# Optimization experiments

Measured on AMD Instinct MI355X. Metric: run time of the kernel, lower is better.

The kernel has to match this reference:

```python
import math
import jax, jax.numpy as jnp
import numpy as np

B, T, N_EMBD, N_HEAD = 1, 16384, 1024, 1
N_ITERS = 30


def setup_inputs() -> dict:
    key = jax.random.key(0)
    kx, kw = jax.random.split(key)
    x = jax.random.normal(kx, (B, T, N_EMBD), dtype=jnp.float32)
    W = jax.random.normal(kw, (2 * N_EMBD + 1, N_EMBD), dtype=jnp.float32) * 0.02
    alpha = jnp.asarray(1.0, dtype=jnp.float32)  # nn.Parameter init
    beta = jnp.asarray(5.0, dtype=jnp.float32)   # nn.Parameter init
    return {"x": x, "W": W, "alpha": alpha, "beta": beta}


def _forward(x, W, alpha, beta):
    Bv, Tv, C = x.shape
    hd = C // N_HEAD
    qkv = x @ W.T                                            # (B,T,2C+1)
    q, k, v = qkv[..., :C], qkv[..., C:2 * C], qkv[..., 2 * C:]
    kh = k.reshape(Bv, Tv, N_HEAD, hd).transpose(0, 2, 1, 3)  # (B,H,T,hd)
    vh = v.reshape(Bv, Tv, N_HEAD, 1).transpose(0, 2, 1, 3)   # (B,H,T,1)
    q_last = q[:, -1].reshape(Bv, N_HEAD, hd)                 # last-token query
    scale = 0.001 / math.sqrt(hd)
    # Only the last query row of the causal attention matrix is consumed;
    # it attends all T keys (causal mask is all-ones on the last row).
    att = jnp.einsum('bhd,bhtd->bht', q_last, kh) * scale     # (B,H,T)
    att = att.at[:, :, -1].set(-jnp.inf)                      # exclude self key
    idx = jnp.arange(Tv)
    counts = (Tv - 1 - idx).astype(att.dtype)                 # distance from end

    def step(carry, _):
        a, b, k_old, done, p = carry
        kk = 2.0 * (a + b) / a                                # truncated window k = 2/p
        window = jnp.ceil(kk)
        mask = idx >= (Tv - window)                           # last `window` keys
        p_new = jax.nn.softmax(jnp.where(mask, att, -jnp.inf), axis=-1)
        bu = jnp.einsum('bht,t->', p_new, counts)             # beta_update (B=H=1 -> scalar)
        a_new, b_new = a + 1.0, b + bu
        done_new = done | (kk > Tv) | (kk < k_old)            # torch break conditions
        k_old_new = jax.lax.stop_gradient(kk)                 # k_old = k.detach()
        keep = lambda old, new: jnp.where(done, old, new)     # freeze after break
        return (keep(a, a_new), keep(b, b_new), keep(k_old, k_old_new),
                done_new, keep(p, p_new)), None

    init = (alpha.astype(att.dtype), beta.astype(att.dtype),
            jnp.asarray(0.0, att.dtype), jnp.asarray(False), jnp.zeros_like(att))
    (_, _, _, _, p), _ = jax.lax.scan(step, init, None, length=N_ITERS)
    # p is zero outside the final window, so the full-length contraction equals
    # att @ v[:, :, -window:, :].
    y = jnp.einsum('bht,bhtd->bhd', p, vh)
    return y.reshape(Bv, 1, 1)


def reference(x, W, alpha, beta):
    return _forward(x, W, alpha, beta)
```

## Files before the change

kernel.cpp:

```cpp
#include <hip/hip_runtime.h>
#include <math.h>

#define T_LEN 16384
#define C_DIM 1024
#define TAIL  256
#define SCAN_ITERS 30


__global__ __launch_bounds__(256)
void k_qw(const float* __restrict__ x, const float* __restrict__ W,
          float* __restrict__ partials) {
    const int tid = threadIdx.x, lane = tid & 63, wid = tid >> 6;
    const int blk = blockIdx.x;
    __shared__ float q_sh[4];

    const float4* xl = (const float4*)(x + (size_t)(T_LEN - 1) * C_DIM);
    const int row = blk * 4 + wid;
    const float4* wq = (const float4*)(W + (size_t)row * C_DIM);
    float acc = 0.f;
#pragma unroll
    for (int it = 0; it < 4; ++it) {
        int idx = lane + 64 * it;
        float4 a = wq[idx];
        float4 b = xl[idx];
        acc += a.x * b.x + a.y * b.y + a.z * b.z + a.w * b.w;
    }
#pragma unroll
    for (int off = 32; off > 0; off >>= 1) acc += __shfl_down(acc, off, 64);
    if (lane == 0) q_sh[wid] = acc;
    __syncthreads();

    const float* Wk = W + (size_t)C_DIM * C_DIM;
    float4 p4 = make_float4(0.f, 0.f, 0.f, 0.f);
#pragma unroll
    for (int r = 0; r < 4; ++r) {
        int ir = blk * 4 + r;
        float4 wkv = ((const float4*)(Wk + (size_t)ir * C_DIM))[tid];
        float qv = q_sh[r];
        p4.x += qv * wkv.x; p4.y += qv * wkv.y;
        p4.z += qv * wkv.z; p4.w += qv * wkv.w;
    }
    ((float4*)(partials + (size_t)blk * C_DIM))[tid] = p4;
}

__global__ __launch_bounds__(256)
void k_red(const float* __restrict__ partials, float* __restrict__ w_eff,
           unsigned int* __restrict__ cnt) {
    const int tid = threadIdx.x, blk = blockIdx.x;
    if (blk == 0 && tid == 0) cnt[0] = 0;
    __shared__ float sh[16][17];
    const int cl = tid & 15, seg = tid >> 4;
    const int col = blk * 16 + cl;
    float s = 0.f;
#pragma unroll
    for (int r = 0; r < 16; ++r)
        s += partials[(size_t)(seg * 16 + r) * C_DIM + col];
    sh[seg][cl] = s;
    __syncthreads();
    if (tid < 16) {
        float t2 = 0.f;
#pragma unroll
        for (int g = 0; g < 16; ++g) t2 += sh[g][tid];
        w_eff[blk * 16 + tid] = t2;
    }
}

__global__ __launch_bounds__(256)
void k_attv(const float* __restrict__ x, const float* __restrict__ W,
            const float* __restrict__ w_eff,
            const float* __restrict__ alpha_p, const float* __restrict__ beta_p,
            unsigned int* __restrict__ cnt,
            float* __restrict__ att, float* __restrict__ v,
            float* __restrict__ out) {
    const int tid = threadIdx.x, lane = tid & 63, wid = tid >> 6;
    const int blk = blockIdx.x;
    __shared__ float redA[4], redV[4];
    __shared__ float red4[4];
    __shared__ float totZ[4], totC[4], totV[4];
    __shared__ float sZ[TAIL], sV[TAIL], sBU[TAIL];
    __shared__ int   last_sh;

    {
        const int t = T_LEN - TAIL + blk;
        const float4* xr = (const float4*)(x + (size_t)t * C_DIM);
        const float4* we = (const float4*)w_eff;
        const float4* wv = (const float4*)(W + (size_t)(2 * C_DIM) * C_DIM);
        float4 a  = xr[tid];
        float4 e  = we[tid];
        float4 bv = wv[tid];
        float accA = a.x * e.x  + a.y * e.y  + a.z * e.z  + a.w * e.w;
        float accV = a.x * bv.x + a.y * bv.y + a.z * bv.z + a.w * bv.w;
#pragma unroll
        for (int off = 32; off > 0; off >>= 1) {
            accA += __shfl_down(accA, off, 64);
            accV += __shfl_down(accV, off, 64);
        }
        if (lane == 0) { redA[wid] = accA; redV[wid] = accV; }
        __syncthreads();
        if (tid == 0) {
            float A = redA[0] + redA[1] + redA[2] + redA[3];
            float V = redV[0] + redV[1] + redV[2] + redV[3];
            const float scale = (float)(0.001 / 32.0);
            att[blk] = (t == T_LEN - 1) ? -INFINITY : A * scale;
            v[blk]   = V;
        }
    }

    __syncthreads();
    if (tid == 0) {
        __threadfence();
        unsigned int ticket = atomicAdd(&cnt[0], 1u);
        last_sh = (ticket == 255u);
    }
    __syncthreads();
    if (!last_sh) return;
    __threadfence();

    const int u = TAIL - 1 - tid;
    const float av = att[u];
    const float vv = v[u];

    float m = av;
#pragma unroll
    for (int off = 32; off > 0; off >>= 1) m = fmaxf(m, __shfl_xor(m, off, 64));
    if (lane == 0) red4[wid] = m;
    __syncthreads();
    m = fmaxf(fmaxf(red4[0], red4[1]), fmaxf(red4[2], red4[3]));

    float e = expf(av - m);
    float c = e * (float)(TAIL - 1 - u);
    float w = e * vv;

    float pz = e, pc = c, pw = w;
#pragma unroll
    for (int off = 1; off < 64; off <<= 1) {
        float tz = __shfl_up(pz, off, 64);
        float tc = __shfl_up(pc, off, 64);
        float tw = __shfl_up(pw, off, 64);
        if (lane >= off) { pz += tz; pc += tc; pw += tw; }
    }
    if (lane == 63) { totZ[wid] = pz; totC[wid] = pc; totV[wid] = pw; }
    __syncthreads();
    {
        float az = 0.f, ac = 0.f, aw = 0.f;
        for (int w2 = 0; w2 < wid; ++w2) { az += totZ[w2]; ac += totC[w2]; aw += totV[w2]; }
        float Zu = pz + az;
        sZ[u]  = Zu;
        sV[u]  = pw + aw;
        sBU[u] = (pc + ac) / Zu;
    }
    __syncthreads();

    if (tid == 0) {
        float a = alpha_p[0], b = beta_p[0], k_old = 0.f;
        int f_start = 0;
        for (int it = 0; it < SCAN_ITERS; ++it) {
            float kk = 2.0f * (a + b) / a;
            float wf = ceilf(kk);
            int start;
            if (wf >= (float)TAIL) start = 0;
            else { int win = (int)wf; start = TAIL - win; if (start < 0) start = 0; }

            float bu = sBU[start];
            f_start = start;
            bool done_next = (kk > (float)T_LEN) || (kk < k_old);
            k_old = kk;
            a += 1.0f;
            b += bu;
            if (done_next) break;
        }
        out[0] = sV[f_start] / sZ[f_start];
    }
}

extern "C" void kernel_launch(void* const* d_in, const int* in_sizes, int n_in,
                              void* d_out, int out_size, void* d_ws, size_t ws_size,
                              hipStream_t stream) {
    const float* x     = (const float*)d_in[0];
    const float* W     = (const float*)d_in[1];
    const float* alpha = (const float*)d_in[2];
    const float* beta  = (const float*)d_in[3];

    float* ws         = (float*)d_ws;
    unsigned int* cnt = (unsigned int*)d_ws;
    float* w_eff      = ws + 16;
    float* att        = w_eff + C_DIM;
    float* v          = att + TAIL;
    float* partials   = v + TAIL;
    float* outp       = (float*)d_out;

    k_qw  <<<256, 256, 0, stream>>>(x, W, partials);
    k_red <<<64,  256, 0, stream>>>(partials, w_eff, cnt);
    k_attv<<<256, 256, 0, stream>>>(x, W, w_eff, alpha, beta, cnt, att, v, outp);
}
```

Baseline: 108.9 us.

## Fuse q/w_eff/attention kernels into one grid with redundant row-group recompute

```diff
diff --git a/kernel.cpp b/kernel.cpp
--- a/kernel.cpp
+++ b/kernel.cpp
@@ -5,104 +5,93 @@
 #define C_DIM 1024
 #define TAIL  256
 #define SCAN_ITERS 30
-
+#define NRG   32
+#define NTG   8
 
 __global__ __launch_bounds__(256)
-void k_qw(const float* __restrict__ x, const float* __restrict__ W,
-          float* __restrict__ partials) {
+void k_fused(const float* __restrict__ x, const float* __restrict__ W,
+             const float* __restrict__ alpha_p, const float* __restrict__ beta_p,
+             unsigned int* __restrict__ cnt,
+             float* __restrict__ attp, float* __restrict__ v,
+             float* __restrict__ out) {
     const int tid = threadIdx.x, lane = tid & 63, wid = tid >> 6;
     const int blk = blockIdx.x;
-    __shared__ float q_sh[4];
+    const int i = blk & 31;
+    const int j = blk >> 5;
+
+    __shared__ float  q_sh[32];
+    __shared__ float4 w_part4[256];
+    __shared__ float  red4[4];
+    __shared__ float  totZ[4], totC[4], totV[4];
+    __shared__ float  sZ[TAIL], sV[TAIL], sBU[TAIL];
+    __shared__ int    last_sh;
 
     const float4* xl = (const float4*)(x + (size_t)(T_LEN - 1) * C_DIM);
-    const int row = blk * 4 + wid;
-    const float4* wq = (const float4*)(W + (size_t)row * C_DIM);
-    float acc = 0.f;
+    float4 xv[4];
 #pragma unroll
-    for (int it = 0; it < 4; ++it) {
-        int idx = lane + 64 * it;
-        float4 a = wq[idx];
-        float4 b = xl[idx];
-        acc += a.x * b.x + a.y * b.y + a.z * b.z + a.w * b.w;
+    for (int it = 0; it < 4; ++it) xv[it] = xl[lane + 64 * it];
+
+    const int R0 = i * 32;
+#pragma unroll
+    for (int rr = 0; rr < 8; ++rr) {
+        const int row = R0 + wid * 8 + rr;
+        const float4* wq = (const float4*)(W + (size_t)row * C_DIM);
+        float acc = 0.f;
+#pragma unroll
+        for (int it = 0; it < 4; ++it) {
+            float4 a = wq[lane + 64 * it];
+            float4 b = xv[it];
+            acc += a.x * b.x + a.y * b.y + a.z * b.z + a.w * b.w;
+        }
+#pragma unroll
+        for (int off = 32; off > 0; off >>= 1) acc += __shfl_down(acc, off, 64);
+        if (lane == 0) q_sh[wid * 8 + rr] = acc;
     }
-#pragma unroll
-    for (int off = 32; off > 0; off >>= 1) acc += __shfl_down(acc, off, 64);
-    if (lane == 0) q_sh[wid] = acc;
     __syncthreads();
 
-    const float* Wk = W + (size_t)C_DIM * C_DIM;
-    float4 p4 = make_float4(0.f, 0.f, 0.f, 0.f);
+    {
+        const float* Wk = W + (size_t)C_DIM * C_DIM;
+        float4 wp = make_float4(0.f, 0.f, 0.f, 0.f);
 #pragma unroll
-    for (int r = 0; r < 4; ++r) {
-        int ir = blk * 4 + r;
-        float4 wkv = ((const float4*)(Wk + (size_t)ir * C_DIM))[tid];
-        float qv = q_sh[r];
-        p4.x += qv * wkv.x; p4.y += qv * wkv.y;
-        p4.z += qv * wkv.z; p4.w += qv * wkv.w;
+        for (int r = 0; r < 32; ++r) {
+            float4 kv = ((const float4*)(Wk + (size_t)(R0 + r) * C_DIM))[tid];
+            float qv = q_sh[r];
+            wp.x += qv * kv.x; wp.y += qv * kv.y;
+            wp.z += qv * kv.z; wp.w += qv * kv.w;
+        }
+        w_part4[tid] = wp;
     }
-    ((float4*)(partials + (size_t)blk * C_DIM))[tid] = p4;
-}
-
-__global__ __launch_bounds__(256)
-void k_red(const float* __restrict__ partials, float* __restrict__ w_eff,
-           unsigned int* __restrict__ cnt) {
-    const int tid = threadIdx.x, blk = blockIdx.x;
-    if (blk == 0 && tid == 0) cnt[0] = 0;
-    __shared__ float sh[16][17];
-    const int cl = tid & 15, seg = tid >> 4;
-    const int col = blk * 16 + cl;
-    float s = 0.f;
-#pragma unroll
-    for (int r = 0; r < 16; ++r)
-        s += partials[(size_t)(seg * 16 + r) * C_DIM + col];
-    sh[seg][cl] = s;
     __syncthreads();
-    if (tid < 16) {
-        float t2 = 0.f;
-#pragma unroll
-        for (int g = 0; g < 16; ++g) t2 += sh[g][tid];
-        w_eff[blk * 16 + tid] = t2;
-    }
-}
-
-__global__ __launch_bounds__(256)
-void k_attv(const float* __restrict__ x, const float* __restrict__ W,
-            const float* __restrict__ w_eff,
-            const float* __restrict__ alpha_p, const float* __restrict__ beta_p,
-            unsigned int* __restrict__ cnt,
-            float* __restrict__ att, float* __restrict__ v,
-            float* __restrict__ out) {
-    const int tid = threadIdx.x, lane = tid & 63, wid = tid >> 6;
-    const int blk = blockIdx.x;
-    __shared__ float redA[4], redV[4];
-    __shared__ float red4[4];
-    __shared__ float totZ[4], totC[4], totV[4];
-    __shared__ float sZ[TAIL], sV[TAIL], sBU[TAIL];
-    __shared__ int   last_sh;
 
     {
-        const int t = T_LEN - TAIL + blk;
-        const float4* xr = (const float4*)(x + (size_t)t * C_DIM);
-        const float4* we = (const float4*)w_eff;
+        const bool do_v = (i == 0);
         const float4* wv = (const float4*)(W + (size_t)(2 * C_DIM) * C_DIM);
-        float4 a  = xr[tid];
-        float4 e  = we[tid];
-        float4 bv = wv[tid];
-        float accA = a.x * e.x  + a.y * e.y  + a.z * e.z  + a.w * e.w;
-        float accV = a.x * bv.x + a.y * bv.y + a.z * bv.z + a.w * bv.w;
 #pragma unroll
-        for (int off = 32; off > 0; off >>= 1) {
-            accA += __shfl_down(accA, off, 64);
-            accV += __shfl_down(accV, off, 64);
-        }
-        if (lane == 0) { redA[wid] = accA; redV[wid] = accV; }
-        __syncthreads();
-        if (tid == 0) {
-            float A = redA[0] + redA[1] + redA[2] + redA[3];
-            float V = redV[0] + redV[1] + redV[2] + redV[3];
-            const float scale = (float)(0.001 / 32.0);
-            att[blk] = (t == T_LEN - 1) ? -INFINITY : A * scale;
-            v[blk]   = V;
+        for (int tt = 0; tt < 8; ++tt) {
+            const int tl = j * 32 + tt * 4 + wid;
+            const int t  = T_LEN - TAIL + tl;
+            const float4* xr = (const float4*)(x + (size_t)t * C_DIM);
+            float accA = 0.f, accV = 0.f;
+#pragma unroll
+            for (int it = 0; it < 4; ++it) {
+                const int idx = lane + 64 * it;
+                float4 a  = xr[idx];
+                float4 wp = w_part4[idx];
+                accA += a.x * wp.x + a.y * wp.y + a.z * wp.z + a.w * wp.w;
+                if (do_v) {
+                    float4 bv = wv[idx];
+                    accV += a.x * bv.x + a.y * bv.y + a.z * bv.z + a.w * bv.w;
+                }
+            }
+#pragma unroll
+            for (int off = 32; off > 0; off >>= 1) {
+                accA += __shfl_down(accA, off, 64);
+                if (do_v) accV += __shfl_down(accV, off, 64);
+            }
+            if (lane == 0) {
+                attp[(size_t)i * TAIL + tl] = accA;
+                if (do_v) v[tl] = accV;
+            }
         }
     }
 
@@ -110,14 +99,18 @@
     if (tid == 0) {
         __threadfence();
         unsigned int ticket = atomicAdd(&cnt[0], 1u);
-        last_sh = (ticket == 255u);
+        last_sh = (ticket == (NRG * NTG - 1));
     }
     __syncthreads();
     if (!last_sh) return;
     __threadfence();
 
     const int u = TAIL - 1 - tid;
-    const float av = att[u];
+    float s = 0.f;
+#pragma unroll
+    for (int k = 0; k < NRG; ++k) s += attp[(size_t)k * TAIL + u];
+    const float scale = (float)(0.001 / 32.0);
+    const float av = (u == TAIL - 1) ? -INFINITY : s * scale;
     const float vv = v[u];
 
     float m = av;
@@ -183,13 +176,11 @@
 
     float* ws         = (float*)d_ws;
     unsigned int* cnt = (unsigned int*)d_ws;
-    float* w_eff      = ws + 16;
-    float* att        = w_eff + C_DIM;
-    float* v          = att + TAIL;
-    float* partials   = v + TAIL;
+    float* attp       = ws + 16;
+    float* v          = attp + (size_t)NRG * TAIL;
     float* outp       = (float*)d_out;
 
-    k_qw  <<<256, 256, 0, stream>>>(x, W, partials);
-    k_red <<<64,  256, 0, stream>>>(partials, w_eff, cnt);
-    k_attv<<<256, 256, 0, stream>>>(x, W, w_eff, alpha, beta, cnt, att, v, outp);
+    hipMemsetAsync(cnt, 0, sizeof(unsigned int), stream);
+    k_fused<<<NRG * NTG, 256, 0, stream>>>(x, W, alpha, beta, cnt,
+                                           attp, v, outp);
 }
```

Result: slower. 118.1 us (+8.4%).
